# Optimization experiments

Measured on AMD Instinct MI355X. Metric: run time of the kernel, lower is better.

Reference implementation:

```python
import jax, jax.numpy as jnp
import numpy as np

N_M = 100000  # musicians
N_T = 100000  # tracks
E = 400000
D = 128


def _sage(x_src, x_dst, edge, W_l, b_l, W_r, n_dst):
    """PyG SAGEConv: lin_l(mean_{j in N(i)} x_src[j]) + lin_r(x_dst[i])."""
    src, dst = edge[0], edge[1]
    msg = x_src[src]                                   # [E, D] gather
    agg = jax.ops.segment_sum(msg, dst, num_segments=n_dst)
    cnt = jax.ops.segment_sum(jnp.ones((edge.shape[1],), x_src.dtype), dst,
                              num_segments=n_dst)
    agg = agg / jnp.maximum(cnt, 1.0)[:, None]         # mean aggregation
    return agg @ W_l.T + b_l + x_dst @ W_r.T


def setup_inputs() -> dict:
    key = jax.random.key(0)
    ks = jax.random.split(key, 7)
    scale = 0.05
    return {
        "x_m": jax.random.normal(ks[0], (N_M, D), jnp.float32),
        "x_t": jax.random.normal(ks[1], (N_T, D), jnp.float32),
        "Wl": jax.random.normal(ks[2], (3, 2, D, D), jnp.float32) * scale,
        "bl": jnp.zeros((3, 2, D), jnp.float32),
        "Wr": jax.random.normal(ks[3], (3, 2, D, D), jnp.float32) * scale,
        "edge_mt": jax.random.randint(ks[4], (2, E), 0, N_T, jnp.int32).astype(jnp.int64),
        "edge_tm": jax.random.randint(ks[5], (2, E), 0, N_M, jnp.int32).astype(jnp.int64),
    }


def reference(x_m, x_t, Wl, bl, Wr, edge_mt, edge_tm):
    # 3 HeteroConv(SAGEConv) layers; dropout=0.0 is identity.
    for layer in range(3):
        # edge type 0: musician -plays_on-> track  (dst = track)
        new_t = _sage(x_m, x_t, edge_mt, Wl[layer, 0], bl[layer, 0], Wr[layer, 0], N_T)
        # edge type 1: track -features-> musician  (dst = musician)
        new_m = _sage(x_t, x_m, edge_tm, Wl[layer, 1], bl[layer, 1], Wr[layer, 1], N_M)
        if layer < 2:
            new_m = jax.nn.relu(new_m)
            new_t = jax.nn.relu(new_t)
        x_m, x_t = new_m, new_t
    return x_m, x_t
```

## Files before the change

### kernel.cpp

```cpp
#include <hip/hip_runtime.h>
#include <hip/hip_bf16.h>

typedef __bf16 bf16_t;
typedef __attribute__((ext_vector_type(4))) __bf16 bf16x4;
typedef __attribute__((ext_vector_type(8))) __bf16 bf16x8;
typedef __attribute__((ext_vector_type(4))) float f32x4;

#define DIM 128
#define GTILE 32

__device__ __forceinline__ void gl_lds16(const void* g, void* l) {
    __builtin_amdgcn_global_load_lds(
        (const __attribute__((address_space(1))) unsigned int*)g,
        (__attribute__((address_space(3))) unsigned int*)l, 16, 0, 0);
}

__global__ void prep_count(const float* __restrict__ Wl, const float* __restrict__ Wr,
                           bf16_t* __restrict__ Wc,
                           const int* __restrict__ dA, int* __restrict__ cA,
                           const int* __restrict__ dB, int* __restrict__ cB, int E,
                           const float* __restrict__ xm, bf16_t* __restrict__ xbm, int CM,
                           const float* __restrict__ xt, bf16_t* __restrict__ xbt, int CT,
                           int PB, int CB) {
    int blk = blockIdx.x;
    if (blk < PB) {
        int idx = blk * 256 + threadIdx.x;
        if (idx >= 6 * 128 * 256) return;
        int k = idx & 255;
        int n = (idx >> 8) & 127;
        int s = idx >> 15;
        float v;
        if (k < 128) v = Wl[((size_t)s * 128 + n) * 128 + k];
        else         v = Wr[((size_t)s * 128 + n) * 128 + (k - 128)];
        Wc[idx] = (bf16_t)v;
    } else if (blk < PB + CB) {
        int i = (blk - PB) * 256 + threadIdx.x;
        if (i < E) atomicAdd(&cA[dA[i]], 1);
        else if (i < 2 * E) atomicAdd(&cB[dB[i - E]], 1);
    } else {
        int i = (blk - PB - CB) * 256 + threadIdx.x;
        const float* src; bf16_t* dst;
        if (i < CM) { src = xm; dst = xbm; }
        else if ((i -= CM) < CT) { src = xt; dst = xbt; }
        else return;
        float4 a = ((const float4*)src)[(size_t)i * 2];
        float4 b = ((const float4*)src)[(size_t)i * 2 + 1];
        bf16x8 r;
        r[0] = (bf16_t)a.x; r[1] = (bf16_t)a.y; r[2] = (bf16_t)a.z; r[3] = (bf16_t)a.w;
        r[4] = (bf16_t)b.x; r[5] = (bf16_t)b.y; r[6] = (bf16_t)b.z; r[7] = (bf16_t)b.w;
        *(bf16x8*)(dst + (size_t)i * 8) = r;
    }
}

__global__ __launch_bounds__(1024) void scan_all(
    const int* __restrict__ cntA, int* __restrict__ rsA, int* __restrict__ curA, int MA,
    const int* __restrict__ cntB, int* __restrict__ rsB, int* __restrict__ curB, int MB) {
    const int* cnt; int* rs; int* cur; int M;
    if (blockIdx.x == 0) { cnt = cntA; rs = rsA; cur = curA; M = MA; }
    else                 { cnt = cntB; rs = rsB; cur = curB; M = MB; }
    __shared__ int swv[16];
    __shared__ int srun;
    const int tid  = threadIdx.x;
    const int wave = tid >> 6;
    const int lane = tid & 63;
    if (tid == 0) srun = 0;
    __syncthreads();
    for (int base = 0; base < M; base += 1024) {
        int i = base + tid;
        int v = (i < M) ? cnt[i] : 0;
        int x = v;
#pragma unroll
        for (int off = 1; off < 64; off <<= 1) {
            int t = __shfl_up(x, off, 64);
            if (lane >= off) x += t;
        }
        if (lane == 63) swv[wave] = x;
        __syncthreads();
        if (wave == 0) {
            int y = (lane < 16) ? swv[lane] : 0;
#pragma unroll
            for (int off = 1; off < 16; off <<= 1) {
                int t = __shfl_up(y, off, 64);
                if (lane >= off) y += t;
            }
            if (lane < 16) swv[lane] = y;
        }
        __syncthreads();
        int r = srun;
        int excl = x - v + (wave ? swv[wave - 1] : 0) + r;
        if (i < M) { rs[i] = excl; cur[i] = excl; }
        __syncthreads();
        if (tid == 0) srun = r + swv[15];
        __syncthreads();
    }
    if (threadIdx.x == 0) rs[M] = srun;
}

__global__ void bin_edges2(const int* __restrict__ sA, const int* __restrict__ dA,
                           int* __restrict__ curA, int* __restrict__ csrA,
                           const int* __restrict__ sB, const int* __restrict__ dB,
                           int* __restrict__ curB, int* __restrict__ csrB, int E) {
    int e = blockIdx.x * blockDim.x + threadIdx.x;
    if (e < E) {
        int d = dA[e];
        int pos = atomicAdd(&curA[d], 1);
        csrA[pos] = sA[e];
    } else if (e < 2 * E) {
        int i = e - E;
        int d = dB[i];
        int pos = atomicAdd(&curB[d], 1);
        csrB[pos] = sB[i];
    }
}

#define A0SZ 8192
#define A1SZ 8192

template <int MODE>
__global__ __launch_bounds__(256, 3) void fused2(
    const bf16_t* __restrict__ gsA, const int* __restrict__ rsA,
    const int* __restrict__ csA,
    const bf16_t* __restrict__ a1A, const bf16_t* __restrict__ WcA,
    const float* __restrict__ bA, void* __restrict__ oA, int Ma,
    const bf16_t* __restrict__ gsB, const int* __restrict__ rsB,
    const int* __restrict__ csB,
    const bf16_t* __restrict__ a1B, const bf16_t* __restrict__ WcB,
    const float* __restrict__ bB, void* __restrict__ oB, int Mb) {
    __shared__ char smem[A0SZ + 2 * A1SZ];

    const int tid  = threadIdx.x;
    const int wid  = tid >> 6;
    const int lane = tid & 63;
    const int quad = lane >> 4;
    const int l16  = lane & 15;

    const int side = blockIdx.x & 1;
    const int t0   = blockIdx.x >> 1;
    const int gs   = gridDim.x >> 1;

    const bf16_t *gsrc, *a1p; const int *rsx, *csx;
    const bf16_t* Wc; const float* bias; void* outp; int M;
    if (side == 0) { gsrc = gsA; rsx = rsA; csx = csA; a1p = a1A;
                     Wc = WcA; bias = bA; outp = oA; M = Ma; }
    else           { gsrc = gsB; rsx = rsB; csx = csB; a1p = a1B;
                     Wc = WcB; bias = bB; outp = oB; M = Mb; }
    const int nt = (M + GTILE - 1) / GTILE;
    if (t0 >= nt) return;

    bf16x8 breg[2][8];
#pragma unroll
    for (int ct = 0; ct < 2; ++ct)
#pragma unroll
        for (int kt = 0; kt < 8; ++kt)
            breg[ct][kt] = *(const bf16x8*)(
                Wc + (size_t)(wid * 32 + ct * 16 + l16) * 256 + kt * 32 + quad * 8);

    const float bcol0 = bias[wid * 32 + l16];
    const float bcol1 = bias[wid * 32 + 16 + l16];
    const int sw = l16 & 7;

    int s_row[2], s_off[2];
#pragma unroll
    for (int c = 0; c < 2; ++c) {
        int o = wid * 2048 + c * 1024 + lane * 16;
        int row = o >> 8;
        int ch  = (o >> 4) & 15;
        s_row[c] = row;
        s_off[c] = (ch ^ (row & 7)) * 8;
    }

    auto STAGE = [&](int b, int t) {
        const int r0 = t * GTILE;
        char* base = smem + A0SZ + b * A1SZ;
#pragma unroll
        for (int c = 0; c < 2; ++c) {
            int grow = r0 + s_row[c]; if (grow >= M) grow = M - 1;
            gl_lds16(a1p + (size_t)grow * DIM + s_off[c],
                     base + wid * 2048 + c * 1024);
        }
    };

    auto GATHER = [&](int t) {
        const int hw  = tid >> 5;
        const int l32 = tid & 31;
        char* a0 = smem;
#pragma unroll
        for (int pr = 0; pr < 2; ++pr) {
            const int r0 = hw * 4 + pr * 2;
            const int r1 = r0 + 1;
            const int d0 = t * GTILE + r0;
            const int d1 = t * GTILE + r1;
            int s0 = 0, n0 = 0, s1 = 0, n1 = 0;
            if (d0 < M) { s0 = rsx[d0]; n0 = rsx[d0 + 1] - s0; }
            if (d1 < M) { s1 = rsx[d1]; n1 = rsx[d1 + 1] - s1; }
            const int b0 = (n0 > 0) ? s0 : 0, lim0 = (n0 > 0) ? n0 - 1 : 0;
            const int b1 = (n1 > 0) ? s1 : 0, lim1 = (n1 > 0) ? n1 - 1 : 0;
            float4 a00 = {0.f,0.f,0.f,0.f}, a01 = {0.f,0.f,0.f,0.f};
            float4 a10 = {0.f,0.f,0.f,0.f}, a11 = {0.f,0.f,0.f,0.f};
            const int nmax = max(n0, n1);
            for (int k = 0; k < nmax; k += 4) {
                int sv0[4], sv1[4];
#pragma unroll
                for (int j = 0; j < 4; ++j) {
                    sv0[j] = csx[b0 + min(k + j, lim0)];
                    sv1[j] = csx[b1 + min(k + j, lim1)];
                }
                bf16x4 v0[4], v1[4];
#pragma unroll
                for (int j = 0; j < 4; ++j)
                    v0[j] = *(const bf16x4*)(gsrc + (size_t)sv0[j] * DIM + l32 * 4);
#pragma unroll
                for (int j = 0; j < 4; ++j)
                    v1[j] = *(const bf16x4*)(gsrc + (size_t)sv1[j] * DIM + l32 * 4);
#pragma unroll
                for (int j = 0; j < 4; j += 2) {
                    float w0 = (k + j     < n0) ? 1.f : 0.f;
                    float w1 = (k + j + 1 < n0) ? 1.f : 0.f;
                    a00.x += (float)v0[j][0] * w0;     a00.y += (float)v0[j][1] * w0;
                    a00.z += (float)v0[j][2] * w0;     a00.w += (float)v0[j][3] * w0;
                    a01.x += (float)v0[j + 1][0] * w1; a01.y += (float)v0[j + 1][1] * w1;
                    a01.z += (float)v0[j + 1][2] * w1; a01.w += (float)v0[j + 1][3] * w1;
                }
#pragma unroll
                for (int j = 0; j < 4; j += 2) {
                    float w0 = (k + j     < n1) ? 1.f : 0.f;
                    float w1 = (k + j + 1 < n1) ? 1.f : 0.f;
                    a10.x += (float)v1[j][0] * w0;     a10.y += (float)v1[j][1] * w0;
                    a10.z += (float)v1[j][2] * w0;     a10.w += (float)v1[j][3] * w0;
                    a11.x += (float)v1[j + 1][0] * w1; a11.y += (float)v1[j + 1][1] * w1;
                    a11.z += (float)v1[j + 1][2] * w1; a11.w += (float)v1[j + 1][3] * w1;
                }
            }
            {
                float invn = 1.0f / (float)max(n0, 1);
                bf16x4 res;
                res[0] = (bf16_t)((a00.x + a01.x) * invn);
                res[1] = (bf16_t)((a00.y + a01.y) * invn);
                res[2] = (bf16_t)((a00.z + a01.z) * invn);
                res[3] = (bf16_t)((a00.w + a01.w) * invn);
                *(bf16x4*)(a0 + r0 * 256 + (((l32 >> 1) ^ (r0 & 7)) << 4) + ((l32 & 1) << 3)) = res;
            }
            {
                float invn = 1.0f / (float)max(n1, 1);
                bf16x4 res;
                res[0] = (bf16_t)((a10.x + a11.x) * invn);
                res[1] = (bf16_t)((a10.y + a11.y) * invn);
                res[2] = (bf16_t)((a10.z + a11.z) * invn);
                res[3] = (bf16_t)((a10.w + a11.w) * invn);
                *(bf16x4*)(a0 + r1 * 256 + (((l32 >> 1) ^ (r1 & 7)) << 4) + ((l32 & 1) << 3)) = res;
            }
        }
    };

    auto COMPUTE = [&](int b, int t) {
        const int r0 = t * GTILE;
        const char* a0base = smem;
        const char* a1base = smem + A0SZ + b * A1SZ;
        f32x4 acc[2][2];
#pragma unroll
        for (int rt = 0; rt < 2; ++rt) {
            acc[rt][0] = (f32x4){0.f, 0.f, 0.f, 0.f};
            acc[rt][1] = (f32x4){0.f, 0.f, 0.f, 0.f};
        }
#pragma unroll
        for (int rt = 0; rt < 2; ++rt) {
            const int row = rt * 16 + l16;
            bf16x8 alo[4];
#pragma unroll
            for (int kt = 0; kt < 4; ++kt)
                alo[kt] = *(const bf16x8*)(a0base + row * 256 + ((kt * 4 + quad) ^ sw) * 16);
#pragma unroll
            for (int kt = 0; kt < 4; ++kt) {
                acc[rt][0] = __builtin_amdgcn_mfma_f32_16x16x32_bf16(alo[kt], breg[0][kt], acc[rt][0], 0, 0, 0);
                acc[rt][1] = __builtin_amdgcn_mfma_f32_16x16x32_bf16(alo[kt], breg[1][kt], acc[rt][1], 0, 0, 0);
            }
#pragma unroll
            for (int kt = 0; kt < 4; ++kt) {
                bf16x8 ah = *(const bf16x8*)(a1base + row * 256 + ((kt * 4 + quad) ^ sw) * 16);
                acc[rt][0] = __builtin_amdgcn_mfma_f32_16x16x32_bf16(ah, breg[0][kt + 4], acc[rt][0], 0, 0, 0);
                acc[rt][1] = __builtin_amdgcn_mfma_f32_16x16x32_bf16(ah, breg[1][kt + 4], acc[rt][1], 0, 0, 0);
            }
        }
#pragma unroll
        for (int ct = 0; ct < 2; ++ct) {
            const int col = wid * 32 + ct * 16 + l16;
            const float bv = ct ? bcol1 : bcol0;
#pragma unroll
            for (int rt = 0; rt < 2; ++rt)
#pragma unroll
                for (int r = 0; r < 4; ++r) {
                    int row = r0 + rt * 16 + quad * 4 + r;
                    if (row < M) {
                        float v = acc[rt][ct][r] + bv;
                        if (MODE == 1) v = fmaxf(v, 0.f);
                        if constexpr (MODE == 2)
                            ((float*)outp)[(size_t)row * DIM + col] = v;
                        else
                            ((bf16_t*)outp)[(size_t)row * DIM + col] = (bf16_t)v;
                    }
                }
        }
    };

    STAGE(0, t0);
    int cur = 0;
    for (int t = t0; t < nt; t += gs, cur ^= 1) {
        const int nxt = t + gs;
        if (nxt < nt) STAGE(cur ^ 1, nxt);
        GATHER(t);
        __syncthreads();
        COMPUTE(cur, t);
        __syncthreads();
    }
}

extern "C" void kernel_launch(void* const* d_in, const int* in_sizes, int n_in,
                              void* d_out, int out_size, void* d_ws, size_t ws_size,
                              hipStream_t stream) {
    const float* x_m = (const float*)d_in[0];
    const float* x_t = (const float*)d_in[1];
    const float* Wl  = (const float*)d_in[2];
    const float* bl  = (const float*)d_in[3];
    const float* Wr  = (const float*)d_in[4];
    const int* e_mt  = (const int*)d_in[5];
    const int* e_tm  = (const int*)d_in[6];

    const int Mm = in_sizes[0] / DIM;
    const int Mt = in_sizes[1] / DIM;
    const int E  = in_sizes[5] / 2;

    float* out_m = (float*)d_out;
    float* out_t = (float*)d_out + (size_t)Mm * DIM;

    char* ws = (char*)d_ws;
    size_t off = 0;
    auto alloc = [&](size_t bytes) -> void* {
        void* p = ws + off;
        off += (bytes + 255) & ~(size_t)255;
        return p;
    };
    bf16_t* xbm    = (bf16_t*)alloc((size_t)Mm * DIM * 2);
    bf16_t* xbt    = (bf16_t*)alloc((size_t)Mt * DIM * 2);
    bf16_t* xb_m0  = (bf16_t*)alloc((size_t)Mm * DIM * 2);
    bf16_t* xb_t0  = (bf16_t*)alloc((size_t)Mt * DIM * 2);
    bf16_t* xb_m1  = (bf16_t*)alloc((size_t)Mm * DIM * 2);
    bf16_t* xb_t1  = (bf16_t*)alloc((size_t)Mt * DIM * 2);
    int*    cnt_t  = (int*)alloc((size_t)Mt * 4);
    int*    cnt_m  = (int*)alloc((size_t)Mm * 4);
    int*    rs_t   = (int*)alloc((size_t)(Mt + 1) * 4);
    int*    rs_m   = (int*)alloc((size_t)(Mm + 1) * 4);
    int*    cur_tb = (int*)alloc((size_t)Mt * 4);
    int*    cur_mb = (int*)alloc((size_t)Mm * 4);
    int*    csr_t  = (int*)alloc((size_t)E * 4);
    int*    csr_m  = (int*)alloc((size_t)E * 4);
    bf16_t* Wc     = (bf16_t*)alloc((size_t)6 * 128 * 256 * 2);

    hipMemsetAsync(cnt_t, 0, (size_t)Mt * 4, stream);
    hipMemsetAsync(cnt_m, 0, (size_t)Mm * 4, stream);

    const int CM = Mm * DIM / 8, CT = Mt * DIM / 8;
    const int PB = (6 * 128 * 256 + 255) / 256;
    const int CB = (2 * E + 255) / 256;
    const int XB = (CM + CT + 255) / 256;
    prep_count<<<PB + CB + XB, 256, 0, stream>>>(Wl, Wr, Wc,
                                                 e_mt + E, cnt_t, e_tm + E, cnt_m, E,
                                                 x_m, xbm, CM, x_t, xbt, CT, PB, CB);

    scan_all<<<2, 1024, 0, stream>>>(cnt_t, rs_t, cur_tb, Mt,
                                     cnt_m, rs_m, cur_mb, Mm);
    bin_edges2<<<(2 * E + 255) / 256, 256, 0, stream>>>(e_mt, e_mt + E, cur_tb, csr_t,
                                                        e_tm, e_tm + E, cur_mb, csr_m, E);

    int GG = 1536;
    {
        int ntT = (Mt + GTILE - 1) / GTILE, ntM = (Mm + GTILE - 1) / GTILE;
        int need = 2 * ((ntT > ntM) ? ntT : ntM);
        if (GG > need) GG = need;
        GG &= ~1;
        if (GG < 2) GG = 2;
    }

    const float* biasT0 = bl + 0 * DIM;  const float* biasM0 = bl + 1 * DIM;
    const float* biasT1 = bl + 2 * DIM;  const float* biasM1 = bl + 3 * DIM;
    const float* biasT2 = bl + 4 * DIM;  const float* biasM2 = bl + 5 * DIM;
    const bf16_t* WcT0 = Wc + 0 * 128 * 256;  const bf16_t* WcM0 = Wc + 1 * 128 * 256;
    const bf16_t* WcT1 = Wc + 2 * 128 * 256;  const bf16_t* WcM1 = Wc + 3 * 128 * 256;
    const bf16_t* WcT2 = Wc + 4 * 128 * 256;  const bf16_t* WcM2 = Wc + 5 * 128 * 256;

    fused2<1><<<GG, 256, 0, stream>>>(
        xbm, rs_t, csr_t, xbt, WcT0, biasT0, xb_t0, Mt,
        xbt, rs_m, csr_m, xbm, WcM0, biasM0, xb_m0, Mm);
    fused2<1><<<GG, 256, 0, stream>>>(
        xb_m0, rs_t, csr_t, xb_t0, WcT1, biasT1, xb_t1, Mt,
        xb_t0, rs_m, csr_m, xb_m0, WcM1, biasM1, xb_m1, Mm);
    fused2<2><<<GG, 256, 0, stream>>>(
        xb_m1, rs_t, csr_t, xb_t1, WcT2, biasT2, out_t, Mt,
        xb_t1, rs_m, csr_m, xb_m1, WcM2, biasM2, out_m, Mm);
}
```

Measured before the change: 594.4 us.

## Replace two-block serial prefix scan with three-phase multi-block scan

The row-offset scan used to run in only two 1024-thread blocks, each walking 100k counts in about 98 serial iterations. It is now split into three kernels: a per-256 block local scan across all blocks, a scan of the block sums, and an offset-add pass. This spreads the scan across the whole GPU, at the cost of two extra kernel launches and extra global traffic for the partial and block-sum arrays. The last row offset is now written as E directly rather than taken from the scan total.

```diff
diff --git a/kernel.cpp b/kernel.cpp
--- a/kernel.cpp
+++ b/kernel.cpp
@@ -52,48 +52,75 @@
     }
 }
 
-__global__ __launch_bounds__(1024) void scan_all(
-    const int* __restrict__ cntA, int* __restrict__ rsA, int* __restrict__ curA, int MA,
-    const int* __restrict__ cntB, int* __restrict__ rsB, int* __restrict__ curB, int MB) {
-    const int* cnt; int* rs; int* cur; int M;
-    if (blockIdx.x == 0) { cnt = cntA; rs = rsA; cur = curA; M = MA; }
-    else                 { cnt = cntB; rs = rsB; cur = curB; M = MB; }
-    __shared__ int swv[16];
-    __shared__ int srun;
-    const int tid  = threadIdx.x;
-    const int wave = tid >> 6;
-    const int lane = tid & 63;
-    if (tid == 0) srun = 0;
+__global__ __launch_bounds__(256) void scan_local2(
+    const int* __restrict__ cntA, int* __restrict__ partA, int* __restrict__ bsumA,
+    int MA, int NBA,
+    const int* __restrict__ cntB, int* __restrict__ partB, int* __restrict__ bsumB,
+    int MB) {
+    int blk = blockIdx.x;
+    const int* cnt; int* partial; int* blocksum; int M; int b;
+    if (blk < NBA) { cnt = cntA; partial = partA; blocksum = bsumA; M = MA; b = blk; }
+    else           { cnt = cntB; partial = partB; blocksum = bsumB; M = MB; b = blk - NBA; }
+    __shared__ int sdata[256];
+    int i = b * 256 + threadIdx.x;
+    int v = (i < M) ? cnt[i] : 0;
+    sdata[threadIdx.x] = v;
     __syncthreads();
-    for (int base = 0; base < M; base += 1024) {
-        int i = base + tid;
-        int v = (i < M) ? cnt[i] : 0;
-        int x = v;
-#pragma unroll
-        for (int off = 1; off < 64; off <<= 1) {
-            int t = __shfl_up(x, off, 64);
-            if (lane >= off) x += t;
-        }
-        if (lane == 63) swv[wave] = x;
-        __syncthreads();
-        if (wave == 0) {
-            int y = (lane < 16) ? swv[lane] : 0;
-#pragma unroll
-            for (int off = 1; off < 16; off <<= 1) {
-                int t = __shfl_up(y, off, 64);
-                if (lane >= off) y += t;
-            }
-            if (lane < 16) swv[lane] = y;
-        }
-        __syncthreads();
-        int r = srun;
-        int excl = x - v + (wave ? swv[wave - 1] : 0) + r;
-        if (i < M) { rs[i] = excl; cur[i] = excl; }
-        __syncthreads();
-        if (tid == 0) srun = r + swv[15];
-        __syncthreads();
-    }
-    if (threadIdx.x == 0) rs[M] = srun;
+    for (int off = 1; off < 256; off <<= 1) {
+        int t = (threadIdx.x >= off) ? sdata[threadIdx.x - off] : 0;
+        __syncthreads();
+        sdata[threadIdx.x] += t;
+        __syncthreads();
+    }
+    int incl = sdata[threadIdx.x];
+    if (i < M) partial[i] = incl - v;
+    if (threadIdx.x == 255) blocksum[b] = incl;
+}
+
+__global__ __launch_bounds__(256) void scan_blocks2(int* __restrict__ bsA, int NA,
+                                                    int* __restrict__ bsB, int NBcnt) {
+    int* blocksum = blockIdx.x ? bsB : bsA;
+    int NB = blockIdx.x ? NBcnt : NA;
+    __shared__ int sdata[256];
+    __shared__ int running;
+    if (threadIdx.x == 0) running = 0;
+    __syncthreads();
+    for (int base = 0; base < NB; base += 256) {
+        int i = base + threadIdx.x;
+        int v = (i < NB) ? blocksum[i] : 0;
+        sdata[threadIdx.x] = v;
+        __syncthreads();
+        for (int off = 1; off < 256; off <<= 1) {
+            int t = (threadIdx.x >= off) ? sdata[threadIdx.x - off] : 0;
+            __syncthreads();
+            sdata[threadIdx.x] += t;
+            __syncthreads();
+        }
+        int incl = sdata[threadIdx.x];
+        int r = running;
+        __syncthreads();
+        if (i < NB) blocksum[i] = incl - v + r;
+        if (threadIdx.x == 0) running = r + sdata[255];
+        __syncthreads();
+    }
+}
+
+__global__ __launch_bounds__(256) void add_offsets2(
+    const int* __restrict__ pA, const int* __restrict__ bsA,
+    int* __restrict__ rsA, int* __restrict__ curA, int MA, int NBA,
+    const int* __restrict__ pB, const int* __restrict__ bsB,
+    int* __restrict__ rsB, int* __restrict__ curB, int MB, int E) {
+    if (blockIdx.x == 0 && threadIdx.x == 0) { rsA[MA] = E; rsB[MB] = E; }
+    int blk = blockIdx.x;
+    const int *partial, *blocksum; int *rowstart, *cursor; int M, b;
+    if (blk < NBA) { partial = pA; blocksum = bsA; rowstart = rsA; cursor = curA; M = MA; b = blk; }
+    else           { partial = pB; blocksum = bsB; rowstart = rsB; cursor = curB; M = MB; b = blk - NBA; }
+    int i = b * 256 + threadIdx.x;
+    if (i < M) {
+        int rs = partial[i] + blocksum[i >> 8];
+        rowstart[i] = rs;
+        cursor[i] = rs;
+    }
 }
 
 __global__ void bin_edges2(const int* __restrict__ sA, const int* __restrict__ dA,
@@ -328,6 +355,8 @@
     const int Mm = in_sizes[0] / DIM;
     const int Mt = in_sizes[1] / DIM;
     const int E  = in_sizes[5] / 2;
+    const int NBt = (Mt + 255) / 256;
+    const int NBm = (Mm + 255) / 256;
 
     float* out_m = (float*)d_out;
     float* out_t = (float*)d_out + (size_t)Mm * DIM;
@@ -351,6 +380,10 @@
     int*    rs_m   = (int*)alloc((size_t)(Mm + 1) * 4);
     int*    cur_tb = (int*)alloc((size_t)Mt * 4);
     int*    cur_mb = (int*)alloc((size_t)Mm * 4);
+    int*    part_t = (int*)alloc((size_t)Mt * 4);
+    int*    part_m = (int*)alloc((size_t)Mm * 4);
+    int*    bsum_t = (int*)alloc((size_t)NBt * 4);
+    int*    bsum_m = (int*)alloc((size_t)NBm * 4);
     int*    csr_t  = (int*)alloc((size_t)E * 4);
     int*    csr_m  = (int*)alloc((size_t)E * 4);
     bf16_t* Wc     = (bf16_t*)alloc((size_t)6 * 128 * 256 * 2);
@@ -366,8 +399,11 @@
                                                  e_mt + E, cnt_t, e_tm + E, cnt_m, E,
                                                  x_m, xbm, CM, x_t, xbt, CT, PB, CB);
 
-    scan_all<<<2, 1024, 0, stream>>>(cnt_t, rs_t, cur_tb, Mt,
-                                     cnt_m, rs_m, cur_mb, Mm);
+    scan_local2<<<NBt + NBm, 256, 0, stream>>>(cnt_t, part_t, bsum_t, Mt, NBt,
+                                               cnt_m, part_m, bsum_m, Mm);
+    scan_blocks2<<<2, 256, 0, stream>>>(bsum_t, NBt, bsum_m, NBm);
+    add_offsets2<<<NBt + NBm, 256, 0, stream>>>(part_t, bsum_t, rs_t, cur_tb, Mt, NBt,
+                                                part_m, bsum_m, rs_m, cur_mb, Mm, E);
     bin_edges2<<<(2 * E + 255) / 256, 256, 0, stream>>>(e_mt, e_mt + E, cur_tb, csr_t,
                                                         e_tm, e_tm + E, cur_mb, csr_m, E);
 
```

New measurement: 503.2 us. 1.18x faster.
